# Performance work log

Hardware: AMD Instinct MI355X
Metric: run time of the kernel (lower is better)

Reference implementation:

```python
import jax, jax.numpy as jnp
import numpy as np

B, S, H, HID, V, NSPEC = 8, 4096, 1024, 128, 60000, 5
EPS = 1e-12
SLOPE = 0.01  # nn.LeakyReLU default negative_slope


def _leaky(x):
    return jnp.where(x >= 0, x, SLOPE * x)


def setup_inputs() -> dict:
    key = jax.random.key(0)
    ks = jax.random.split(key, 12)
    gene_ids = jax.random.randint(ks[0], (B, S), 0, V)
    cont = jax.random.uniform(ks[1], (B, S), jnp.float32, 0.0, 10.0)
    spec_mask = jax.random.uniform(ks[2], (B, S)) < 0.05
    spec_vals = -jax.random.randint(ks[3], (B, S), 1, NSPEC + 1).astype(jnp.float32)
    expr_values = jnp.where(spec_mask, spec_vals, cont)
    gene_emb = jax.random.normal(ks[4], (V, H), jnp.float32) * 0.02
    W1 = jax.random.normal(ks[5], (HID,), jnp.float32) * 0.5   # Linear(1,128) weight
    b1 = jax.random.normal(ks[6], (HID,), jnp.float32) * 0.1
    W2 = jax.random.normal(ks[7], (HID, H), jnp.float32) * 0.05  # Linear(128,H)
    b2 = jax.random.normal(ks[8], (H,), jnp.float32) * 0.1
    special_emb = jax.random.normal(ks[9], (NSPEC, HID), jnp.float32) * 0.02
    special_emb = special_emb.at[2].set(0.0)  # padding_idx=2
    pos_emb = jax.random.normal(ks[10], (S, H), jnp.float32) * 0.02
    gamma = jnp.ones((H,), jnp.float32)
    beta = jnp.zeros((H,), jnp.float32)
    return dict(gene_ids=gene_ids, expr_values=expr_values, gene_emb=gene_emb,
                W1=W1, b1=b1, W2=W2, b2=b2, special_emb=special_emb,
                pos_emb=pos_emb, gamma=gamma, beta=beta)


def reference(gene_ids, expr_values, gene_emb, W1, b1, W2, b2, special_emb,
              pos_emb, gamma, beta):
    x = expr_values                                  # [B,S]
    special = x < 0                                  # special-token mask
    # mapped special id: -(int(x)+1); clamp so gather is in-range on non-special slots
    mapped = jnp.clip(-(x.astype(jnp.int32) + 1), 0, NSPEC - 1)
    spec_e = special_emb[mapped]                     # [B,S,HID] gather
    cont_e = _leaky(x[..., None] * W1 + b1)          # dense_1 on scalar value
    h = jnp.where(special[..., None], spec_e, cont_e)  # scatter-combine
    expr_e = _leaky(h) @ W2 + b2                     # dense_2 -> [B,S,H]
    emb = gene_emb[gene_ids] + expr_e + pos_emb[None, :, :]
    mu = jnp.mean(emb, axis=-1, keepdims=True)
    var = jnp.mean(jnp.square(emb - mu), axis=-1, keepdims=True)
    out = (emb - mu) * jax.lax.rsqrt(var + EPS) * gamma + beta
    return out  # dropout is identity at inference (p used at train only)
```

## Files before the change

kernel.cpp:

```cpp
#include <hip/hip_runtime.h>
#include <hip/hip_bf16.h>

#define B_DIM   8
#define S_LEN   4096
#define H_DIM   1024
#define HID_DIM 128
#define NSPEC   5
#define NROWS   (HID_DIM + 1 + NSPEC)
#define SLOPE   0.01f
#define LN_EPS  1e-12f
#define FUSE_GRID 2048

typedef float vfloat4 __attribute__((ext_vector_type(4)));

__global__ __launch_bounds__(256) void build_kernel(
        const float* __restrict__ W1,
        const float* __restrict__ b1,
        const float* __restrict__ W2,
        const float* __restrict__ b2,
        const float* __restrict__ spec,
        float* __restrict__ tvals,
        float2* __restrict__ tab) {
    const int row = blockIdx.x;
    const int tid = threadIdx.x;

    __shared__ float tsh[HID_DIM];
    __shared__ float ash[HID_DIM];
    __shared__ float csh[HID_DIM];

    float w = 0.0f, b = 0.0f, t = 0.0f;
    if (tid < HID_DIM) {
        w = W1[tid];
        b = b1[tid];
        t = (w != 0.0f) ? (-b / w) : __builtin_inff();
        tsh[tid] = t;
        if (row == 0) tvals[tid] = t;
    }
    __syncthreads();
    if (tid < HID_DIM) {
        int r = 0;
        #pragma unroll 8
        for (int k2 = 0; k2 < HID_DIM; ++k2) {
            const float t2 = tsh[k2];
            if (t2 < t || (t2 == t && k2 < tid)) ++r;
        }

        float a, c;
        if (row <= HID_DIM) {
            const bool crossed = (r < row);
            bool zpos;
            if (w > 0.0f)      zpos = crossed;
            else if (w < 0.0f) zpos = !crossed;
            else               zpos = (b >= 0.0f);
            const float s = zpos ? 1.0f : (SLOPE * SLOPE);
            a = s * w;
            c = s * b;
        } else {
            const int m = row - (HID_DIM + 1);
            const float e = spec[m * HID_DIM + tid];
            a = 0.0f;
            c = (e >= 0.0f) ? e : SLOPE * e;
        }
        ash[tid] = a;
        csh[tid] = c;
    }
    __syncthreads();

    float4 u = make_float4(0.f, 0.f, 0.f, 0.f);
    float4 v = make_float4(0.f, 0.f, 0.f, 0.f);
    #pragma unroll 4
    for (int k = 0; k < HID_DIM; ++k) {
        const float4 w2 = reinterpret_cast<const float4*>(W2 + (size_t)k * H_DIM)[tid];
        const float a = ash[k], c = csh[k];
        u.x = fmaf(a, w2.x, u.x);  v.x = fmaf(c, w2.x, v.x);
        u.y = fmaf(a, w2.y, u.y);  v.y = fmaf(c, w2.y, v.y);
        u.z = fmaf(a, w2.z, u.z);  v.z = fmaf(c, w2.z, v.z);
        u.w = fmaf(a, w2.w, u.w);  v.w = fmaf(c, w2.w, v.w);
    }
    const float4 bb = reinterpret_cast<const float4*>(b2)[tid];
    float4* trow = reinterpret_cast<float4*>(tab + (size_t)row * H_DIM);
    trow[2 * tid]     = make_float4(u.x, v.x + bb.x, u.y, v.y + bb.y);
    trow[2 * tid + 1] = make_float4(u.z, v.z + bb.z, u.w, v.w + bb.w);
}

__global__ __launch_bounds__(256, 4) void fuse_kernel(
        const int*   __restrict__ gene_ids,
        const float* __restrict__ expr,
        const float* __restrict__ gene_emb,
        const float* __restrict__ pos_emb,
        const float* __restrict__ gamma,
        const float* __restrict__ beta,
        const float* __restrict__ tvals,
        const float2* __restrict__ tab,
        float* __restrict__ out,
        int ngroups) {
    const int tid  = threadIdx.x;
    const int lane = tid & 63;
    const int wv   = tid >> 6;

    __shared__ float4 gm_lds[H_DIM / 4];
    __shared__ float4 bt_lds[H_DIM / 4];
    gm_lds[tid] = reinterpret_cast<const float4*>(gamma)[tid];
    bt_lds[tid] = reinterpret_cast<const float4*>(beta)[tid];

    const float tka = tvals[lane];
    const float tkb = tvals[lane + 64];

    const int t_first = blockIdx.x * 4 + wv;
    const int sp      = t_first & (S_LEN - 1);
    const float4* pp  = reinterpret_cast<const float4*>(pos_emb + (size_t)sp * H_DIM);
    float4 p[4];
    #pragma unroll
    for (int q = 0; q < 4; ++q) p[q] = pp[lane + 64 * q];

    __syncthreads();

    float x   = expr[t_first];
    int   gid = gene_ids[t_first];

    for (int grp = blockIdx.x; grp < ngroups; grp += gridDim.x) {
        const int t = grp * 4 + wv;

        const int tn = t + 4 * gridDim.x;
        float nx  = 0.0f;
        int   ngid = 0;
        if (tn < 4 * ngroups) {
            nx   = expr[tn];
            ngid = gene_ids[tn];
        }

        const float4* gp = reinterpret_cast<const float4*>(gene_emb + (size_t)gid * H_DIM);
        float4 g[4];
        #pragma unroll
        for (int q = 0; q < 4; ++q) g[q] = gp[lane + 64 * q];

        const int rc = __popcll(__ballot(tka <= x)) + __popcll(__ballot(tkb <= x));
        const bool spc = (x < 0.0f);
        const int  msp = min(max(-((int)x) - 1, 0), NSPEC - 1);
        const int  row = spc ? (HID_DIM + 1 + msp) : rc;
        const float xm = spc ? 0.0f : x;

        const float4* tp = reinterpret_cast<const float4*>(tab + (size_t)row * H_DIM);
        float4 ta[4], tb[4];
        #pragma unroll
        for (int q = 0; q < 4; ++q) {
            const int f = lane + 64 * q;
            ta[q] = tp[2 * f];
            tb[q] = tp[2 * f + 1];
        }

        float4 e[4];
        float s1 = 0.0f, s2 = 0.0f;
        #pragma unroll
        for (int q = 0; q < 4; ++q) {
            float4 ev;
            ev.x = g[q].x + fmaf(xm, ta[q].x, ta[q].y) + p[q].x;
            ev.y = g[q].y + fmaf(xm, ta[q].z, ta[q].w) + p[q].y;
            ev.z = g[q].z + fmaf(xm, tb[q].x, tb[q].y) + p[q].z;
            ev.w = g[q].w + fmaf(xm, tb[q].z, tb[q].w) + p[q].w;
            e[q] = ev;
            s1 += ev.x + ev.y + ev.z + ev.w;
            s2 += ev.x * ev.x + ev.y * ev.y + ev.z * ev.z + ev.w * ev.w;
        }

        #pragma unroll
        for (int off = 32; off >= 1; off >>= 1) {
            s1 += __shfl_xor(s1, off, 64);
            s2 += __shfl_xor(s2, off, 64);
        }

        const float inv  = 1.0f / (float)H_DIM;
        const float mu   = s1 * inv;
        const float rsig = rsqrtf(s2 * inv - mu * mu + LN_EPS);

        vfloat4* op = reinterpret_cast<vfloat4*>(out + (size_t)t * H_DIM);
        #pragma unroll
        for (int q = 0; q < 4; ++q) {
            const int f = lane + 64 * q;
            const float4 gm = gm_lds[f];
            const float4 bt = bt_lds[f];
            vfloat4 o;
            o.x = fmaf((e[q].x - mu) * rsig, gm.x, bt.x);
            o.y = fmaf((e[q].y - mu) * rsig, gm.y, bt.y);
            o.z = fmaf((e[q].z - mu) * rsig, gm.z, bt.z);
            o.w = fmaf((e[q].w - mu) * rsig, gm.w, bt.w);
            __builtin_nontemporal_store(o, op + f);
        }

        x   = nx;
        gid = ngid;
    }
}

extern "C" void kernel_launch(void* const* d_in, const int* in_sizes, int n_in,
                              void* d_out, int out_size, void* d_ws, size_t ws_size,
                              hipStream_t stream) {
    const int*   gene_ids = (const int*)  d_in[0];
    const float* expr     = (const float*)d_in[1];
    const float* gene_emb = (const float*)d_in[2];
    const float* W1       = (const float*)d_in[3];
    const float* b1       = (const float*)d_in[4];
    const float* W2       = (const float*)d_in[5];
    const float* b2       = (const float*)d_in[6];
    const float* spec     = (const float*)d_in[7];
    const float* pos_emb  = (const float*)d_in[8];
    const float* gamma    = (const float*)d_in[9];
    const float* beta     = (const float*)d_in[10];
    float* out = (float*)d_out;

    const size_t tab_bytes = (size_t)NROWS * H_DIM * sizeof(float2);
    float2* tab   = (float2*)d_ws;
    float*  tvals = (float*)((char*)d_ws + tab_bytes);

    const int n_tokens = in_sizes[0];
    const int ngroups  = n_tokens / 4;

    build_kernel<<<NROWS, 256, 0, stream>>>(W1, b1, W2, b2, spec, tvals, tab);
    fuse_kernel<<<FUSE_GRID, 256, 0, stream>>>(gene_ids, expr, gene_emb, pos_emb,
                                               gamma, beta, tvals, tab, out, ngroups);
}
```

Before: 67.89 us.

## Assign each wave one sequence position across the batch and prefetch the next token

Each wave now owns one sequence position and loops over all 8 batch entries, so the positional embedding row is loaded once and reused every iteration. The gene embedding and table rows for the next token are software-pipelined one iteration ahead, with ids and values fetched two ahead. The grid becomes a fixed 1024 blocks and launch bounds drop to 2 blocks per SM, which allows more registers for the double-buffered data but lowers occupancy. The code now hardcodes the batch count through NITER and S_LEN, so it assumes n_tokens equals B*S.

```diff
diff --git a/kernel.cpp b/kernel.cpp
--- a/kernel.cpp
+++ b/kernel.cpp
@@ -9,7 +9,7 @@
 #define NROWS   (HID_DIM + 1 + NSPEC)
 #define SLOPE   0.01f
 #define LN_EPS  1e-12f
-#define FUSE_GRID 2048
+#define NITER   8
 
 typedef float vfloat4 __attribute__((ext_vector_type(4)));
 
@@ -83,7 +83,7 @@
     trow[2 * tid + 1] = make_float4(u.z, v.z + bb.z, u.w, v.w + bb.w);
 }
 
-__global__ __launch_bounds__(256, 4) void fuse_kernel(
+__global__ __launch_bounds__(256, 2) void fuse_kernel(
         const int*   __restrict__ gene_ids,
         const float* __restrict__ expr,
         const float* __restrict__ gene_emb,
@@ -92,11 +92,10 @@
         const float* __restrict__ beta,
         const float* __restrict__ tvals,
         const float2* __restrict__ tab,
-        float* __restrict__ out,
-        int ngroups) {
+        float* __restrict__ out) {
     const int tid  = threadIdx.x;
     const int lane = tid & 63;
-    const int wv   = tid >> 6;
+    const int w    = blockIdx.x * 4 + (tid >> 6);
 
     __shared__ float4 gm_lds[H_DIM / 4];
     __shared__ float4 bt_lds[H_DIM / 4];
@@ -105,48 +104,65 @@
 
     const float tka = tvals[lane];
     const float tkb = tvals[lane + 64];
-
-    const int t_first = blockIdx.x * 4 + wv;
-    const int sp      = t_first & (S_LEN - 1);
-    const float4* pp  = reinterpret_cast<const float4*>(pos_emb + (size_t)sp * H_DIM);
+    const float4* pp = reinterpret_cast<const float4*>(pos_emb + (size_t)w * H_DIM);
     float4 p[4];
     #pragma unroll
     for (int q = 0; q < 4; ++q) p[q] = pp[lane + 64 * q];
 
     __syncthreads();
 
-    float x   = expr[t_first];
-    int   gid = gene_ids[t_first];
-
-    for (int grp = blockIdx.x; grp < ngroups; grp += gridDim.x) {
-        const int t = grp * 4 + wv;
-
-        const int tn = t + 4 * gridDim.x;
-        float nx  = 0.0f;
-        int   ngid = 0;
-        if (tn < 4 * ngroups) {
-            nx   = expr[tn];
-            ngid = gene_ids[tn];
-        }
-
-        const float4* gp = reinterpret_cast<const float4*>(gene_emb + (size_t)gid * H_DIM);
-        float4 g[4];
-        #pragma unroll
-        for (int q = 0; q < 4; ++q) g[q] = gp[lane + 64 * q];
-
-        const int rc = __popcll(__ballot(tka <= x)) + __popcll(__ballot(tkb <= x));
-        const bool spc = (x < 0.0f);
-        const int  msp = min(max(-((int)x) - 1, 0), NSPEC - 1);
-        const int  row = spc ? (HID_DIM + 1 + msp) : rc;
-        const float xm = spc ? 0.0f : x;
-
+    float x_c  = expr[w];
+    int   gd_c = gene_ids[w];
+    float x_n  = expr[w + S_LEN];
+    int   gd_n = gene_ids[w + S_LEN];
+
+    float xm_c;
+    float4 g_c[4], ta_c[4], tb_c[4];
+    {
+        const int rc = __popcll(__ballot(tka <= x_c)) + __popcll(__ballot(tkb <= x_c));
+        const bool sc = (x_c < 0.0f);
+        const int  mc = min(max(-((int)x_c) - 1, 0), NSPEC - 1);
+        const int  row = sc ? (HID_DIM + 1 + mc) : rc;
+        xm_c = sc ? 0.0f : x_c;
+        const float4* gp = reinterpret_cast<const float4*>(gene_emb + (size_t)gd_c * H_DIM);
         const float4* tp = reinterpret_cast<const float4*>(tab + (size_t)row * H_DIM);
-        float4 ta[4], tb[4];
         #pragma unroll
         for (int q = 0; q < 4; ++q) {
             const int f = lane + 64 * q;
-            ta[q] = tp[2 * f];
-            tb[q] = tp[2 * f + 1];
+            g_c[q]  = gp[f];
+            ta_c[q] = tp[2 * f];
+            tb_c[q] = tp[2 * f + 1];
+        }
+    }
+
+    #pragma unroll 8
+    for (int i = 0; i < NITER; ++i) {
+        const int t = w + i * S_LEN;
+
+        float x_n2  = 0.0f;
+        int   gd_n2 = 0;
+        if (i + 2 < NITER) {
+            x_n2  = expr[t + 2 * S_LEN];
+            gd_n2 = gene_ids[t + 2 * S_LEN];
+        }
+
+        float xm_n = 0.0f;
+        float4 g_n[4], ta_n[4], tb_n[4];
+        if (i + 1 < NITER) {
+            const int rc = __popcll(__ballot(tka <= x_n)) + __popcll(__ballot(tkb <= x_n));
+            const bool sn = (x_n < 0.0f);
+            const int  mn = min(max(-((int)x_n) - 1, 0), NSPEC - 1);
+            const int  rown = sn ? (HID_DIM + 1 + mn) : rc;
+            xm_n = sn ? 0.0f : x_n;
+            const float4* gp = reinterpret_cast<const float4*>(gene_emb + (size_t)gd_n * H_DIM);
+            const float4* tp = reinterpret_cast<const float4*>(tab + (size_t)rown * H_DIM);
+            #pragma unroll
+            for (int q = 0; q < 4; ++q) {
+                const int f = lane + 64 * q;
+                g_n[q]  = gp[f];
+                ta_n[q] = tp[2 * f];
+                tb_n[q] = tp[2 * f + 1];
+            }
         }
 
         float4 e[4];
@@ -154,10 +170,10 @@
         #pragma unroll
         for (int q = 0; q < 4; ++q) {
             float4 ev;
-            ev.x = g[q].x + fmaf(xm, ta[q].x, ta[q].y) + p[q].x;
-            ev.y = g[q].y + fmaf(xm, ta[q].z, ta[q].w) + p[q].y;
-            ev.z = g[q].z + fmaf(xm, tb[q].x, tb[q].y) + p[q].z;
-            ev.w = g[q].w + fmaf(xm, tb[q].z, tb[q].w) + p[q].w;
+            ev.x = g_c[q].x + fmaf(xm_c, ta_c[q].x, ta_c[q].y) + p[q].x;
+            ev.y = g_c[q].y + fmaf(xm_c, ta_c[q].z, ta_c[q].w) + p[q].y;
+            ev.z = g_c[q].z + fmaf(xm_c, tb_c[q].x, tb_c[q].y) + p[q].z;
+            ev.w = g_c[q].w + fmaf(xm_c, tb_c[q].z, tb_c[q].w) + p[q].w;
             e[q] = ev;
             s1 += ev.x + ev.y + ev.z + ev.w;
             s2 += ev.x * ev.x + ev.y * ev.y + ev.z * ev.z + ev.w * ev.w;
@@ -187,8 +203,15 @@
             __builtin_nontemporal_store(o, op + f);
         }
 
-        x   = nx;
-        gid = ngid;
+        xm_c = xm_n;
+        x_n  = x_n2;
+        gd_n = gd_n2;
+        #pragma unroll
+        for (int q = 0; q < 4; ++q) {
+            g_c[q]  = g_n[q];
+            ta_c[q] = ta_n[q];
+            tb_c[q] = tb_n[q];
+        }
     }
 }
 
@@ -213,9 +236,9 @@
     float*  tvals = (float*)((char*)d_ws + tab_bytes);
 
     const int n_tokens = in_sizes[0];
-    const int ngroups  = n_tokens / 4;
+    const int nwaves   = n_tokens / NITER;
 
     build_kernel<<<NROWS, 256, 0, stream>>>(W1, b1, W2, b2, spec, tvals, tab);
-    fuse_kernel<<<FUSE_GRID, 256, 0, stream>>>(gene_ids, expr, gene_emb, pos_emb,
-                                               gamma, beta, tvals, tab, out, ngroups);
+    fuse_kernel<<<nwaves / 4, 256, 0, stream>>>(gene_ids, expr, gene_emb, pos_emb,
+                                                gamma, beta, tvals, tab, out);
 }
```

Measured after the change: 64.75 us. 4.6% less time.
